# Performance work log

Measured on AMD Instinct MI355X. Metric: run time of the kernel, lower is better.

Reference implementation:

```python
import jax, jax.numpy as jnp
import numpy as np

N_NODES = 100000
N_EDGES = 1600000
N_GRAPHS = 64
D = 128          # input_features == hidden_sf*model_dim == out_sf*output_channels
N_CLASSES = 10   # out_dim
N_LAYERS = 3


def setup_inputs() -> dict:
    key = jax.random.key(0)
    ks = jax.random.split(key, 8)
    x = jax.random.normal(ks[0], (N_NODES, D), dtype=jnp.float32)
    edge_index = jax.random.randint(ks[1], (2, N_EDGES), 0, N_NODES, dtype=jnp.int64)
    batch = jnp.sort(jax.random.randint(ks[2], (N_NODES,), 0, N_GRAPHS, dtype=jnp.int64))
    s = 1.0 / np.sqrt(D)
    # PyG GraphConv: out = lin_rel(aggr(x_j)) + lin_root(x); lin_root has no bias
    W_rel = jax.random.uniform(ks[3], (N_LAYERS, D, D), jnp.float32, -s, s)
    W_root = jax.random.uniform(ks[4], (N_LAYERS, D, D), jnp.float32, -s, s)
    b_rel = jax.random.uniform(ks[5], (N_LAYERS, D), jnp.float32, -s, s)
    W_fc = jax.random.uniform(ks[6], (D, N_CLASSES), jnp.float32, -s, s)
    b_fc = jax.random.uniform(ks[7], (N_CLASSES,), jnp.float32, -s, s)
    return dict(x=x, edge_index=edge_index, batch=batch,
                W_rel=W_rel, W_root=W_root, b_rel=b_rel, W_fc=W_fc, b_fc=b_fc)


def reference(x, edge_index, batch, W_rel, W_root, b_rel, W_fc, b_fc):
    src, dst = edge_index[0], edge_index[1]  # messages flow src -> dst
    for i in range(N_LAYERS):  # small fixed layer count
        agg = jax.ops.segment_sum(x[src], dst, num_segments=N_NODES)  # [N, D] gather+scatter-add
        x = agg @ W_rel[i] + b_rel[i] + x @ W_root[i]
    # global mean pool over graphs
    counts = jax.ops.segment_sum(jnp.ones((N_NODES,), x.dtype), batch, num_segments=N_GRAPHS)
    pooled = jax.ops.segment_sum(x, batch, num_segments=N_GRAPHS) / jnp.maximum(counts, 1.0)[:, None]
    logits = pooled @ W_fc + b_fc  # [N_GRAPHS, N_CLASSES]
    return jax.nn.log_softmax(logits, axis=1)
```

## Files before the change

### kernel.cpp

```cpp
#include <hip/hip_runtime.h>
#include <hip/hip_bf16.h>

#define D 128
#define NGRAPHS 64
#define NCLASSES 10
#define NB 800
#define CAP 3072
#define EPB 8192

typedef unsigned short u16;
typedef unsigned int u32;
typedef __attribute__((ext_vector_type(8))) short bf16x8;
typedef __attribute__((ext_vector_type(4))) float f32x4;

__device__ __forceinline__ u16 rne_bf16(float f) {
  u32 u = __float_as_uint(f);
  u += 0x7FFFu + ((u >> 16) & 1u);
  return (u16)(u >> 16);
}
__device__ __forceinline__ float bf_lo(u32 u) { return __uint_as_float(u << 16); }
__device__ __forceinline__ float bf_hi(u32 u) { return __uint_as_float(u & 0xFFFF0000u); }

__device__ __forceinline__ void gload_lds16(const void* g, void* l) {
  __builtin_amdgcn_global_load_lds(
      (const __attribute__((address_space(1))) void*)g,
      (__attribute__((address_space(3))) void*)l, 16, 0, 0);
}

__global__ __launch_bounds__(256) void k_cast0(const float* __restrict__ x,
                                               u16* __restrict__ xb, long long n8) {
  long long i = (long long)blockIdx.x * 256 + threadIdx.x;
  if (i >= n8) return;
  const float4* xp = reinterpret_cast<const float4*>(x) + i * 2;
  float4 a = xp[0], b = xp[1];
  u32 w0 = rne_bf16(a.x) | ((u32)rne_bf16(a.y) << 16);
  u32 w1 = rne_bf16(a.z) | ((u32)rne_bf16(a.w) << 16);
  u32 w2 = rne_bf16(b.x) | ((u32)rne_bf16(b.y) << 16);
  u32 w3 = rne_bf16(b.z) | ((u32)rne_bf16(b.w) << 16);
  reinterpret_cast<uint4*>(xb)[i] = make_uint4(w0, w1, w2, w3);
}

__global__ __launch_bounds__(256) void k_prep_wt(const float* __restrict__ W_rel,
                                                 const float* __restrict__ W_root,
                                                 u16* __restrict__ Wt) {
  int id = blockIdx.x * 256 + threadIdx.x;
  if (id >= 6 * D * D) return;
  int col = id & 127;
  int k = (id >> 7) & 127;
  int m = id >> 14;
  const float* src = (m < 3) ? (W_rel + (size_t)m * D * D) : (W_root + (size_t)(m - 3) * D * D);
  Wt[(size_t)m * D * D + col * D + k] = rne_bf16(src[k * D + col]);
}

__global__ __launch_bounds__(256) void k_bin(
    const int* __restrict__ src, const int* __restrict__ dst,
    int* __restrict__ gcnt, u32* __restrict__ ebuf, int n_edges, int nb) {
  __shared__ int lh[NB];
  int tid = threadIdx.x;
  int e0 = blockIdx.x * EPB;
  for (int b = tid; b < NB; b += 256) lh[b] = 0;
  __syncthreads();
  for (int i = tid; i < EPB; i += 256) {
    int e = e0 + i;
    if (e < n_edges) atomicAdd(&lh[dst[e] >> 7], 1);
  }
  __syncthreads();
  for (int b = tid; b < nb; b += 256) {
    int c = lh[b];
    lh[b] = (c > 0) ? (b * CAP + atomicAdd(&gcnt[b], c)) : 0;
  }
  __syncthreads();
  for (int i = tid; i < EPB; i += 256) {
    int e = e0 + i;
    if (e < n_edges) {
      int d = dst[e];
      int slot = atomicAdd(&lh[d >> 7], 1);
      ebuf[slot] = ((u32)(d & 127) << 20) | (u32)src[e];
    }
  }
}

__global__ __launch_bounds__(256) void k_sort(
    const u32* __restrict__ ebuf, const int* __restrict__ gcnt,
    u32* __restrict__ eidx, int* __restrict__ rowptr, int* __restrict__ deg,
    int n_nodes) {
  __shared__ u32 earr[CAP];
  __shared__ int lh[128], sc[128], lcur[128];
  int tid = threadIdx.x;
  int b = blockIdx.x;
  int cnt = gcnt[b];
  int base = b * CAP;
  for (int i = tid; i < cnt; i += 256) earr[i] = ebuf[base + i];
  if (tid < 128) lh[tid] = 0;
  __syncthreads();
  for (int i = tid; i < cnt; i += 256) atomicAdd(&lh[earr[i] >> 20], 1);
  __syncthreads();
  if (tid < 128) sc[tid] = lh[tid];
  __syncthreads();
  #pragma unroll
  for (int off = 1; off < 128; off <<= 1) {
    int v = (tid < 128 && tid >= off) ? sc[tid - off] : 0;
    __syncthreads();
    if (tid < 128) sc[tid] += v;
    __syncthreads();
  }
  if (tid < 128) {
    int excl = sc[tid] - lh[tid];
    int n = b * 128 + tid;
    if (n < n_nodes) { rowptr[n] = base + excl; deg[n] = lh[tid]; }
    lcur[tid] = excl;
  }
  __syncthreads();
  for (int i = tid; i < cnt; i += 256) {
    u32 e = earr[i];
    int slot = atomicAdd(&lcur[e >> 20], 1);
    eidx[base + slot] = e & 0xFFFFF;
  }
}

__global__ __launch_bounds__(256) void k_gather(
    const u16* __restrict__ xb, const int* __restrict__ rowptr,
    const int* __restrict__ deg, const u32* __restrict__ eidx,
    u16* __restrict__ aggb, int n_nodes) {
  int tid = threadIdx.x;
  int lane = tid & 63;
  int n = blockIdx.x * 4 + (tid >> 6);
  if (n >= n_nodes) return;
  int es = lane >> 4;
  int c = lane & 15;
  int beg = rowptr[n];
  int dn = deg[n];
  float a0 = 0, a1 = 0, a2 = 0, a3 = 0, a4 = 0, a5 = 0, a6 = 0, a7 = 0;
  int i = 0;
  for (; i + 8 <= dn; i += 8) {
    int s0 = (int)eidx[beg + i + es];
    int s1 = (int)eidx[beg + i + 4 + es];
    uint4 v0 = *(reinterpret_cast<const uint4*>(xb + (size_t)s0 * D) + c);
    uint4 v1 = *(reinterpret_cast<const uint4*>(xb + (size_t)s1 * D) + c);
    a0 += bf_lo(v0.x) + bf_lo(v1.x); a1 += bf_hi(v0.x) + bf_hi(v1.x);
    a2 += bf_lo(v0.y) + bf_lo(v1.y); a3 += bf_hi(v0.y) + bf_hi(v1.y);
    a4 += bf_lo(v0.z) + bf_lo(v1.z); a5 += bf_hi(v0.z) + bf_hi(v1.z);
    a6 += bf_lo(v0.w) + bf_lo(v1.w); a7 += bf_hi(v0.w) + bf_hi(v1.w);
  }
  for (; i < dn; i += 4) {
    bool p = (i + es) < dn;
    int s = p ? (int)eidx[beg + i + es] : 0;
    if (p) {
      uint4 v = *(reinterpret_cast<const uint4*>(xb + (size_t)s * D) + c);
      a0 += bf_lo(v.x); a1 += bf_hi(v.x);
      a2 += bf_lo(v.y); a3 += bf_hi(v.y);
      a4 += bf_lo(v.z); a5 += bf_hi(v.z);
      a6 += bf_lo(v.w); a7 += bf_hi(v.w);
    }
  }
  #pragma unroll
  for (int d = 16; d <= 32; d <<= 1) {
    a0 += __shfl_xor(a0, d); a1 += __shfl_xor(a1, d);
    a2 += __shfl_xor(a2, d); a3 += __shfl_xor(a3, d);
    a4 += __shfl_xor(a4, d); a5 += __shfl_xor(a5, d);
    a6 += __shfl_xor(a6, d); a7 += __shfl_xor(a7, d);
  }
  if (es == 0) {
    u32 w0 = rne_bf16(a0) | ((u32)rne_bf16(a1) << 16);
    u32 w1 = rne_bf16(a2) | ((u32)rne_bf16(a3) << 16);
    u32 w2 = rne_bf16(a4) | ((u32)rne_bf16(a5) << 16);
    u32 w3 = rne_bf16(a6) | ((u32)rne_bf16(a7) << 16);
    *(reinterpret_cast<uint4*>(aggb + (size_t)n * D) + c) = make_uint4(w0, w1, w2, w3);
  }
}

__global__ __launch_bounds__(256) void k_gemm_mfma(
    const u16* __restrict__ A1, const u16* __restrict__ A2,
    const u16* __restrict__ Wt1, const u16* __restrict__ Wt2,
    const float* __restrict__ bias, u16* __restrict__ outp, int M) {
  __shared__ __align__(16) u16 As[2][128 * 64];
  __shared__ __align__(16) u16 Ws[2][128 * 64];
  int tid = threadIdx.x;
  int wave = tid >> 6, lane = tid & 63;
  int g = lane >> 4, lr = lane & 15;
  int r0 = blockIdx.x * 128;
  int wr = wave * 32;

  f32x4 acc[2][8];
  #pragma unroll
  for (int fr = 0; fr < 2; fr++)
    #pragma unroll
    for (int fc = 0; fc < 8; fc++)
      acc[fr][fc] = (f32x4){0.f, 0.f, 0.f, 0.f};

  const u16* Am[2] = {A1, A2};
  const u16* Wm[2] = {Wt1, Wt2};

  auto STAGE = [&](int buf, const u16* A, const u16* Wt, int kh) {
    #pragma unroll
    for (int i = 0; i < 4; i++) {
      int gI = i * 256 + tid;
      int row = gI >> 3;
      int cs = (gI & 7) ^ (row & 7);
      int rg = r0 + row; if (rg >= M) rg = M - 1;
      u16* la = &As[buf][(size_t)(i * 256 + wave * 64) * 8];
      gload_lds16(A + (size_t)rg * D + kh * 64 + cs * 8, la);
      u16* lw = &Ws[buf][(size_t)(i * 256 + wave * 64) * 8];
      gload_lds16(Wt + (size_t)row * D + kh * 64 + cs * 8, lw);
    }
  };

  STAGE(0, A1, Wt1, 0);
  __syncthreads();

  #pragma unroll 1
  for (int s = 0; s < 4; s++) {
    if (s < 3) {
      int ns = s + 1;
      STAGE(ns & 1, Am[ns >> 1], Wm[ns >> 1], ns & 1);
    }
    int buf = s & 1;
    #pragma unroll
    for (int kc = 0; kc < 2; kc++) {
      int kbyte = kc * 64 + g * 16;
      bf16x8 af[2];
      #pragma unroll
      for (int fr = 0; fr < 2; fr++) {
        int row = wr + fr * 16 + lr;
        int ob = (kbyte ^ ((row & 7) << 4)) >> 1;
        af[fr] = *reinterpret_cast<const bf16x8*>(&As[buf][row * 64 + ob]);
      }
      #pragma unroll
      for (int fc = 0; fc < 8; fc++) {
        int colw = fc * 16 + lr;
        int ob = (kbyte ^ ((colw & 7) << 4)) >> 1;
        bf16x8 bfv = *reinterpret_cast<const bf16x8*>(&Ws[buf][colw * 64 + ob]);
        #pragma unroll
        for (int fr = 0; fr < 2; fr++)
          acc[fr][fc] = __builtin_amdgcn_mfma_f32_16x16x32_bf16(
              af[fr], bfv, acc[fr][fc], 0, 0, 0);
      }
    }
    __syncthreads();
  }

  #pragma unroll
  for (int fc = 0; fc < 8; fc++) {
    float bc = bias[fc * 16 + lr];
    #pragma unroll
    for (int fr = 0; fr < 2; fr++) {
      #pragma unroll
      for (int j = 0; j < 4; j++) {
        int R = r0 + wr + fr * 16 + g * 4 + j;
        if (R < M)
          outp[(size_t)R * D + fc * 16 + lr] = rne_bf16(acc[fr][fc][j] + bc);
      }
    }
  }
}

__global__ __launch_bounds__(256) void k_poolhead(
    const u16* __restrict__ xb, const int* __restrict__ batch,
    const float* __restrict__ W_fc, const float* __restrict__ b_fc,
    float* __restrict__ outp, int n_nodes) {
  __shared__ float pp[16][128];
  __shared__ float lg[128][NCLASSES];
  int tid = threadIdx.x;
  int g = blockIdx.x;
  int rs = tid >> 4, c = tid & 15;

  int lo = 0, hi = n_nodes;
  while (lo < hi) { int m = (lo + hi) >> 1; if (batch[m] < g) lo = m + 1; else hi = m; }
  int start = lo;
  hi = n_nodes;
  while (lo < hi) { int m = (lo + hi) >> 1; if (batch[m] < g + 1) lo = m + 1; else hi = m; }
  int end = lo;
  int cnt = end - start;

  float a0 = 0, a1 = 0, a2 = 0, a3 = 0, a4 = 0, a5 = 0, a6 = 0, a7 = 0;
  for (int r = start + rs; r < end; r += 16) {
    uint4 v = *(reinterpret_cast<const uint4*>(xb + (size_t)r * D) + c);
    a0 += bf_lo(v.x); a1 += bf_hi(v.x);
    a2 += bf_lo(v.y); a3 += bf_hi(v.y);
    a4 += bf_lo(v.z); a5 += bf_hi(v.z);
    a6 += bf_lo(v.w); a7 += bf_hi(v.w);
  }
  pp[rs][c * 8 + 0] = a0; pp[rs][c * 8 + 1] = a1;
  pp[rs][c * 8 + 2] = a2; pp[rs][c * 8 + 3] = a3;
  pp[rs][c * 8 + 4] = a4; pp[rs][c * 8 + 5] = a5;
  pp[rs][c * 8 + 6] = a6; pp[rs][c * 8 + 7] = a7;
  __syncthreads();
  for (int s = 8; s >= 1; s >>= 1) {
    if (rs < s) {
      #pragma unroll
      for (int j = 0; j < 8; j++) pp[rs][c * 8 + j] += pp[rs + s][c * 8 + j];
    }
    __syncthreads();
  }
  float inv = 1.0f / fmaxf((float)cnt, 1.0f);
  if (tid < 128) {
    float p = pp[0][tid] * inv;
    #pragma unroll
    for (int j = 0; j < NCLASSES; j++) lg[tid][j] = p * W_fc[tid * NCLASSES + j];
  }
  __syncthreads();
  for (int s = 64; s >= 1; s >>= 1) {
    if (tid < s) {
      #pragma unroll
      for (int j = 0; j < NCLASSES; j++) lg[tid][j] += lg[tid + s][j];
    }
    __syncthreads();
  }
  if (tid == 0) {
    float logits[NCLASSES];
    #pragma unroll
    for (int j = 0; j < NCLASSES; j++) logits[j] = lg[0][j] + b_fc[j];
    float m = logits[0];
    #pragma unroll
    for (int j = 1; j < NCLASSES; j++) m = fmaxf(m, logits[j]);
    float s2 = 0.f;
    #pragma unroll
    for (int j = 0; j < NCLASSES; j++) s2 += expf(logits[j] - m);
    float lse = m + logf(s2);
    #pragma unroll
    for (int j = 0; j < NCLASSES; j++) outp[g * NCLASSES + j] = logits[j] - lse;
  }
}

extern "C" void kernel_launch(void* const* d_in, const int* in_sizes, int n_in,
                              void* d_out, int out_size, void* d_ws, size_t ws_size,
                              hipStream_t stream) {
  const float* x      = (const float*)d_in[0];
  const int*   ei     = (const int*)d_in[1];
  const int*   batch  = (const int*)d_in[2];
  const float* W_rel  = (const float*)d_in[3];
  const float* W_root = (const float*)d_in[4];
  const float* b_rel  = (const float*)d_in[5];
  const float* W_fc   = (const float*)d_in[6];
  const float* b_fc   = (const float*)d_in[7];
  float* outp = (float*)d_out;

  int n_nodes = in_sizes[0] / D;
  int n_edges = in_sizes[1] / 2;
  const int* src = ei;
  const int* dst = ei + n_edges;
  int nb = (n_nodes + 127) / 128;

  char* ws = (char*)d_ws;
  size_t bb = (size_t)n_nodes * D * sizeof(u16);
  size_t nbts = (size_t)n_nodes * sizeof(int);
  u16* aggb   = (u16*)(ws);
  u16* xba    = (u16*)(ws + bb);
  u16* xbb    = (u16*)(ws + 2 * bb);
  char* p     = ws + 3 * bb;
  u16* Wt     = (u16*)(p);               p += (size_t)6 * D * D * sizeof(u16);
  int* gcnt   = (int*)(p);               p += (size_t)NB * sizeof(int);
  u32* ebuf   = (u32*)(p);               p += (size_t)NB * CAP * sizeof(u32);
  u32* eidx   = (u32*)(p);               p += (size_t)NB * CAP * sizeof(u32);
  int* rowptr = (int*)(p);               p += nbts;
  int* deg    = (int*)(p);               p += nbts;

  k_prep_wt<<<(6 * D * D + 255) / 256, 256, 0, stream>>>(W_rel, W_root, Wt);
  long long n8 = (long long)n_nodes * D / 8;
  k_cast0<<<(int)((n8 + 255) / 256), 256, 0, stream>>>(x, xba, n8);
  hipMemsetAsync(gcnt, 0, (size_t)NB * sizeof(int), stream);
  k_bin<<<(n_edges + EPB - 1) / EPB, 256, 0, stream>>>(src, dst, gcnt, ebuf, n_edges, nb);
  k_sort<<<nb, 256, 0, stream>>>(ebuf, gcnt, eidx, rowptr, deg, n_nodes);

  u16* xc = xba;
  u16* xn = xbb;
  int gemmblk = (n_nodes + 127) / 128;
  for (int l = 0; l < 3; l++) {
    k_gather<<<(n_nodes + 3) / 4, 256, 0, stream>>>(xc, rowptr, deg, eidx, aggb, n_nodes);
    k_gemm_mfma<<<gemmblk, 256, 0, stream>>>(
        aggb, xc, Wt + (size_t)l * D * D, Wt + (size_t)(3 + l) * D * D,
        b_rel + (size_t)l * D, xn, n_nodes);
    u16* t = xc; xc = xn; xn = t;
  }

  k_poolhead<<<NGRAPHS, 256, 0, stream>>>(xc, batch, W_fc, b_fc, outp, n_nodes);
}
```

Before: 468.2 us.

## Single-buffer GEMM LDS tiles, add wave priority, fold gcnt memset into weight prep

The GEMM kernel drops LDS double buffering. It now loads each K-stage into a single As/Ws tile, synchronises, then computes, with s_setprio raised around the MFMA section. This halves LDS use per block so more blocks can be resident per CU, but it gives up overlap of global-to-LDS loads with compute inside a block. Separately, the hipMemsetAsync of the bin counters is folded into the k_prep_wt kernel to remove one stream operation.

```diff
diff --git a/kernel.cpp b/kernel.cpp
--- a/kernel.cpp
+++ b/kernel.cpp
@@ -42,7 +42,11 @@
 
 __global__ __launch_bounds__(256) void k_prep_wt(const float* __restrict__ W_rel,
                                                  const float* __restrict__ W_root,
-                                                 u16* __restrict__ Wt) {
+                                                 u16* __restrict__ Wt,
+                                                 int* __restrict__ gcnt) {
+  if (blockIdx.x == 0) {
+    for (int b = threadIdx.x; b < NB; b += 256) gcnt[b] = 0;
+  }
   int id = blockIdx.x * 256 + threadIdx.x;
   if (id >= 6 * D * D) return;
   int col = id & 127;
@@ -173,8 +177,8 @@
     const u16* __restrict__ A1, const u16* __restrict__ A2,
     const u16* __restrict__ Wt1, const u16* __restrict__ Wt2,
     const float* __restrict__ bias, u16* __restrict__ outp, int M) {
-  __shared__ __align__(16) u16 As[2][128 * 64];
-  __shared__ __align__(16) u16 Ws[2][128 * 64];
+  __shared__ __align__(16) u16 As[128 * 64];
+  __shared__ __align__(16) u16 Ws[128 * 64];
   int tid = threadIdx.x;
   int wave = tid >> 6, lane = tid & 63;
   int g = lane >> 4, lr = lane & 15;
@@ -191,30 +195,24 @@
   const u16* Am[2] = {A1, A2};
   const u16* Wm[2] = {Wt1, Wt2};
 
-  auto STAGE = [&](int buf, const u16* A, const u16* Wt, int kh) {
+  #pragma unroll 1
+  for (int s = 0; s < 4; s++) {
+    const u16* A = Am[s >> 1];
+    const u16* Wt = Wm[s >> 1];
+    int kh = s & 1;
     #pragma unroll
     for (int i = 0; i < 4; i++) {
       int gI = i * 256 + tid;
       int row = gI >> 3;
       int cs = (gI & 7) ^ (row & 7);
       int rg = r0 + row; if (rg >= M) rg = M - 1;
-      u16* la = &As[buf][(size_t)(i * 256 + wave * 64) * 8];
+      u16* la = &As[(size_t)(i * 256 + wave * 64) * 8];
       gload_lds16(A + (size_t)rg * D + kh * 64 + cs * 8, la);
-      u16* lw = &Ws[buf][(size_t)(i * 256 + wave * 64) * 8];
+      u16* lw = &Ws[(size_t)(i * 256 + wave * 64) * 8];
       gload_lds16(Wt + (size_t)row * D + kh * 64 + cs * 8, lw);
     }
-  };
-
-  STAGE(0, A1, Wt1, 0);
-  __syncthreads();
-
-  #pragma unroll 1
-  for (int s = 0; s < 4; s++) {
-    if (s < 3) {
-      int ns = s + 1;
-      STAGE(ns & 1, Am[ns >> 1], Wm[ns >> 1], ns & 1);
-    }
-    int buf = s & 1;
+    __syncthreads();
+    __builtin_amdgcn_s_setprio(1);
     #pragma unroll
     for (int kc = 0; kc < 2; kc++) {
       int kbyte = kc * 64 + g * 16;
@@ -223,19 +221,20 @@
       for (int fr = 0; fr < 2; fr++) {
         int row = wr + fr * 16 + lr;
         int ob = (kbyte ^ ((row & 7) << 4)) >> 1;
-        af[fr] = *reinterpret_cast<const bf16x8*>(&As[buf][row * 64 + ob]);
+        af[fr] = *reinterpret_cast<const bf16x8*>(&As[row * 64 + ob]);
       }
       #pragma unroll
       for (int fc = 0; fc < 8; fc++) {
         int colw = fc * 16 + lr;
         int ob = (kbyte ^ ((colw & 7) << 4)) >> 1;
-        bf16x8 bfv = *reinterpret_cast<const bf16x8*>(&Ws[buf][colw * 64 + ob]);
+        bf16x8 bfv = *reinterpret_cast<const bf16x8*>(&Ws[colw * 64 + ob]);
         #pragma unroll
         for (int fr = 0; fr < 2; fr++)
           acc[fr][fc] = __builtin_amdgcn_mfma_f32_16x16x32_bf16(
               af[fr], bfv, acc[fr][fc], 0, 0, 0);
       }
     }
+    __builtin_amdgcn_s_setprio(0);
     __syncthreads();
   }
 
@@ -355,10 +354,9 @@
   int* rowptr = (int*)(p);               p += nbts;
   int* deg    = (int*)(p);               p += nbts;
 
-  k_prep_wt<<<(6 * D * D + 255) / 256, 256, 0, stream>>>(W_rel, W_root, Wt);
+  k_prep_wt<<<(6 * D * D + 255) / 256, 256, 0, stream>>>(W_rel, W_root, Wt, gcnt);
   long long n8 = (long long)n_nodes * D / 8;
   k_cast0<<<(int)((n8 + 255) / 256), 256, 0, stream>>>(x, xba, n8);
-  hipMemsetAsync(gcnt, 0, (size_t)NB * sizeof(int), stream);
   k_bin<<<(n_edges + EPB - 1) / EPB, 256, 0, stream>>>(src, dst, gcnt, ebuf, n_edges, nb);
   k_sort<<<nb, 256, 0, stream>>>(ebuf, gcnt, eidx, rowptr, deg, n_nodes);
 
```

Measured after the change: 478.0 us. 1.02x slower.
